# Kernel tuning notes

Hardware: AMD Instinct MI355X
Metric: run time of the kernel (lower is better)

Reference implementation:

```python
import jax, jax.numpy as jnp
import numpy as np

D_IN = 784
D = 768          # hidden_dim
R = 8            # num_rels
L = 3            # num_layers
B = 64           # graphs in batch
N = 32768        # total nodes
E = 262144       # total edges


def _layer_norm(x, g, b, eps=1e-5):
    m = x.mean(-1, keepdims=True)
    v = x.var(-1, keepdims=True)
    return (x - m) / jnp.sqrt(v + eps) * g + b


def setup_inputs() -> dict:
    key = jax.random.key(0)
    ks = jax.random.split(key, 24)
    s = 0.02
    inp = {
        "type_vec": jax.random.normal(ks[0], (N, 16), jnp.float32),
        "code_vec": jax.random.normal(ks[1], (N, D), jnp.float32),
        # input_proj: Linear(784,768) + LayerNorm(768)
        "W_in": jax.random.normal(ks[2], (D_IN, D), jnp.float32) * s,
        "b_in": jnp.zeros((D,), jnp.float32),
        "ln_in_g": jnp.ones((D,), jnp.float32),
        "ln_in_b": jnp.zeros((D,), jnp.float32),
        # RGCN layers (basis regularizer, num_bases=num_rels -> per-relation W)
        "W_rel": jax.random.normal(ks[3], (L, R, D, D), jnp.float32) * s,
        "W_loop": jax.random.normal(ks[4], (L, D, D), jnp.float32) * s,
        "rgcn_bias": jnp.zeros((L, D), jnp.float32),
        "ln_g": jnp.ones((L, D), jnp.float32),
        "ln_b": jnp.zeros((L, D), jnp.float32),
        # global attention pooling gate MLP: 768 -> 384 -> 1
        "Wg1": jax.random.normal(ks[5], (D, D // 2), jnp.float32) * s,
        "bg1": jnp.zeros((D // 2,), jnp.float32),
        "Wg2": jax.random.normal(ks[6], (D // 2, 1), jnp.float32) * s,
        "bg2": jnp.zeros((1,), jnp.float32),
        # classifier: 768 -> 512 (+LN) -> 2
        "Wc1": jax.random.normal(ks[7], (D, 512), jnp.float32) * s,
        "bc1": jnp.zeros((512,), jnp.float32),
        "ln_c_g": jnp.ones((512,), jnp.float32),
        "ln_c_b": jnp.zeros((512,), jnp.float32),
        "Wc2": jax.random.normal(ks[8], (512, 2), jnp.float32) * s,
        "bc2": jnp.zeros((2,), jnp.float32),
        # graph structure
        "src": jax.random.randint(ks[9], (E,), 0, N, jnp.int64),
        "dst": jax.random.randint(ks[10], (E,), 0, N, jnp.int64),
        "edge_type": jax.random.randint(ks[11], (E,), 0, R, jnp.int64),
        "node_graph": jnp.sort(jax.random.randint(ks[12], (N,), 0, B, jnp.int64)),
        "num_graphs": B,
    }
    return inp


def reference(type_vec, code_vec, W_in, b_in, ln_in_g, ln_in_b,
              W_rel, W_loop, rgcn_bias, ln_g, ln_b,
              Wg1, bg1, Wg2, bg2, Wc1, bc1, ln_c_g, ln_c_b, Wc2, bc2,
              src, dst, edge_type, node_graph, num_graphs):
    # input projection
    h = jnp.concatenate([type_vec, code_vec], axis=-1)           # [N, 784]
    h = jax.nn.gelu(_layer_norm(h @ W_in + b_in, ln_in_g, ln_in_b), approximate=False)
    n_nodes = h.shape[0]
    n_layers, n_rels = W_rel.shape[0], W_rel.shape[1]

    for l in range(n_layers):
        agg = jnp.zeros_like(h)
        for r in range(n_rels):
            # relation-specific transform, then gather->mask->scatter-add
            msg = (h @ W_rel[l, r])[src] * (edge_type == r).astype(h.dtype)[:, None]  # [E, D]
            agg = agg + jax.ops.segment_sum(msg, dst, num_segments=n_nodes)
        h_new = agg + rgcn_bias[l] + h @ W_loop[l]               # DGL: agg + bias + self-loop
        h = jax.nn.gelu(_layer_norm(h_new, ln_g[l], ln_b[l]), approximate=False)

    # global attention pooling (segment softmax over nodes of each graph)
    gate = (jax.nn.gelu(h @ Wg1 + bg1, approximate=False) @ Wg2 + bg2)[:, 0]  # [N]
    gmax = jax.ops.segment_max(gate, node_graph, num_segments=num_graphs)
    e = jnp.exp(gate - gmax[node_graph])
    denom = jax.ops.segment_sum(e, node_graph, num_segments=num_graphs)
    w = e / denom[node_graph]
    graph_repr = jax.ops.segment_sum(w[:, None] * h, node_graph, num_segments=num_graphs)  # [B, D]

    # classifier head
    z = jax.nn.gelu(_layer_norm(graph_repr @ Wc1 + bc1, ln_c_g, ln_c_b), approximate=False)
    logits = z @ Wc2 + bc2
    return jax.nn.log_softmax(logits, axis=-1)
```

## Files before the change

### kernel.cpp

```cpp
#include <hip/hip_runtime.h>
#include <hip/hip_bf16.h>

typedef __hip_bfloat16 bf16;
typedef __attribute__((ext_vector_type(8))) __bf16 bf16x8;
typedef __attribute__((ext_vector_type(4))) float f32x4;

#define N_NODES 32768
#define N_EDGES 262144
#define DIM 768
#define NGR 64
#define KIN 800
#define KSTACK 6912
#define NKEY (N_NODES * 8)

#define GLOBAL_AS __attribute__((address_space(1)))
#define LDS_AS __attribute__((address_space(3)))

__device__ __forceinline__ float gelu_f(float x) {
    return 0.5f * x * (1.0f + erff(x * 0.70710678118654752f));
}
__device__ __forceinline__ float bfu(unsigned short v) {
    union { unsigned u; float f; } x; x.u = (unsigned)v << 16; return x.f;
}
__device__ __forceinline__ unsigned short fbf(float f) {
    bf16 t = __float2bfloat16(f); return *(unsigned short*)&t;
}

__global__ __launch_bounds__(256)
void tcast_k(const float* __restrict__ in, bf16* __restrict__ out, int I, int O,
             int Ipad, int ostride) {
    __shared__ float t[32][33];
    const int i0 = blockIdx.x * 32, o0 = blockIdx.y * 32;
    const int tx = threadIdx.x & 31, ty = threadIdx.x >> 5;
#pragma unroll
    for (int q = 0; q < 4; ++q) {
        int i = i0 + ty + q * 8, o = o0 + tx;
        t[ty + q * 8][tx] = (i < I) ? in[(size_t)i * O + o] : 0.0f;
    }
    __syncthreads();
#pragma unroll
    for (int q = 0; q < 4; ++q) {
        int o = o0 + ty + q * 8, i = i0 + tx;
        if (i < Ipad) out[(size_t)o * ostride + i] = __float2bfloat16(t[tx][ty + q * 8]);
    }
}

__global__ __launch_bounds__(256)
void wprep_l_k(const float* __restrict__ Wrel_l, const float* __restrict__ Wloop_l,
               bf16* __restrict__ WstL) {
    __shared__ float t[32][33];
    const int q = blockIdx.z;
    const float* in = (q < 8) ? Wrel_l + (size_t)q * DIM * DIM : Wloop_l;
    bf16* out = WstL + (q < 8 ? (q + 1) * DIM : 0);
    const int i0 = blockIdx.x * 32, o0 = blockIdx.y * 32;
    const int tx = threadIdx.x & 31, ty = threadIdx.x >> 5;
#pragma unroll
    for (int qq = 0; qq < 4; ++qq)
        t[ty + qq * 8][tx] = in[(size_t)(i0 + ty + qq * 8) * DIM + o0 + tx];
    __syncthreads();
#pragma unroll
    for (int qq = 0; qq < 4; ++qq)
        out[(size_t)(o0 + ty + qq * 8) * KSTACK + i0 + tx] =
            __float2bfloat16(t[tx][ty + qq * 8]);
}

__global__ __launch_bounds__(256)
void concat_k(const float* __restrict__ tv, const float* __restrict__ cv, bf16* __restrict__ X) {
    const int n = blockIdx.x;
    for (int c = threadIdx.x; c < KIN; c += 256) {
        float v = 0.0f;
        if (c < 16) v = tv[(size_t)n * 16 + c];
        else if (c < 784) v = cv[(size_t)n * DIM + (c - 16)];
        X[(size_t)n * KIN + c] = __float2bfloat16(v);
    }
}

__global__ __launch_bounds__(256)
void hist2_k(const int* __restrict__ dst, const int* __restrict__ et, int* __restrict__ cur) {
    int e = blockIdx.x * 256 + threadIdx.x;
    if (e < N_EDGES) atomicAdd(&cur[dst[e] * 8 + et[e]], 1);
}

__global__ __launch_bounds__(1024)
void scan2_k(int* __restrict__ cur, int* __restrict__ rp) {
    __shared__ int part[1024];
    const int t = threadIdx.x;
    const int base_i = t * 256;
    int s = 0;
    for (int i = 0; i < 256; ++i) s += cur[base_i + i];
    part[t] = s; __syncthreads();
    for (int st = 1; st < 1024; st <<= 1) {
        int v = (t >= st) ? part[t - st] : 0;
        __syncthreads();
        part[t] += v;
        __syncthreads();
    }
    int run = part[t] - s;
    for (int i = 0; i < 256; ++i) {
        int d = cur[base_i + i];
        rp[base_i + i] = run; cur[base_i + i] = run;
        run += d;
    }
    if (t == 1023) rp[NKEY] = run;
}

__global__ __launch_bounds__(256)
void place2_k(const int* __restrict__ src, const int* __restrict__ dst,
              const int* __restrict__ et, int* __restrict__ cur,
              unsigned short* __restrict__ eidx) {
    int e = blockIdx.x * 256 + threadIdx.x;
    if (e >= N_EDGES) return;
    int pos = atomicAdd(&cur[dst[e] * 8 + et[e]], 1);
    eidx[pos] = (unsigned short)src[e];
}

template <int NC>
__global__ __launch_bounds__(256)
void gather2_k(const bf16* __restrict__ h, const int* __restrict__ rp2,
               const unsigned short* __restrict__ eidx, bf16* __restrict__ AGG,
               int rbase, int ostride, int colbase) {
    const int wave = threadIdx.x >> 6, lane = threadIdx.x & 63;
    const int n = blockIdx.x * 4 + wave;
    const int c0 = 2 * lane;
    unsigned short* outrow = (unsigned short*)&AGG[(size_t)n * ostride + colbase];
    const int* bp = &rp2[n * 8 + rbase];
#pragma unroll 1
    for (int sel = 0; sel < NC; ++sel) {
        const int s = bp[sel], e = bp[sel + 1];
        float2 f[6] = {};
        for (int t = s; t < e; ++t) {
            const unsigned short* hs = (const unsigned short*)&h[(size_t)eidx[t] * DIM];
#pragma unroll
            for (int j = 0; j < 6; ++j) {
                ushort2 u = *(const ushort2*)&hs[c0 + j * 128];
                f[j].x += bfu(u.x); f[j].y += bfu(u.y);
            }
        }
#pragma unroll
        for (int j = 0; j < 6; ++j) {
            ushort2 o; o.x = fbf(f[j].x); o.y = fbf(f[j].y);
            *(ushort2*)&outrow[sel * DIM + c0 + j * 128] = o;
        }
    }
}

template <int MODE>
__global__ __launch_bounds__(512, 4)
void gemm256(const bf16* __restrict__ A1, int S1, int K1,
             const bf16* __restrict__ A2, int S2,
             const bf16* __restrict__ BT, int ldb,
             bf16* __restrict__ OUT, int Nn, int Ktot, int nbx) {
    __shared__ __align__(16) unsigned short lA[3][128 * 32];
    __shared__ __align__(16) unsigned short lB[3][256 * 32];
    const int nblk = gridDim.x, qx = nblk >> 3, bid = blockIdx.x;
    const int wgid = (bid & 7) * qx + (bid >> 3);
    const int bx = wgid % nbx, by = wgid / nbx;
    const int bn = bx * 256, bm = by * 128;
    const int tid = threadIdx.x;
    const int wave = tid >> 6, lane = tid & 63;
    const int wr = wave >> 2, wc = wave & 3;
    const int l15 = lane & 15, lg = lane >> 4;
    const int swz = (lg ^ ((l15 >> 1) & 3)) * 8;

    f32x4 acc[4][4] = {};
    const int nkt = Ktot >> 5;

    auto stage = [&](int t, int buf) {
        const int k0 = t * 32;
        const bf16* Ab; int koff, stA;
        if (k0 < K1) { Ab = A1; koff = k0; stA = S1; }
        else         { Ab = A2; koff = k0 - K1; stA = S2; }
        {
            const int row = tid >> 2, k8 = tid & 3;
            const int ks = (k8 ^ ((row >> 1) & 3)) * 8;
            const bf16* ga = Ab + (size_t)(bm + row) * stA + koff + ks;
            __builtin_amdgcn_global_load_lds((const GLOBAL_AS void*)ga,
                (LDS_AS void*)&lA[buf][(wave * 64) * 8], 16, 0, 0);
        }
#pragma unroll
        for (int qq = 0; qq < 2; ++qq) {
            const int c = qq * 512 + tid;
            const int row = c >> 2, k8 = c & 3;
            const int ks = (k8 ^ ((row >> 1) & 3)) * 8;
            const bf16* gb = BT + (size_t)(bn + row) * ldb + k0 + ks;
            __builtin_amdgcn_global_load_lds((const GLOBAL_AS void*)gb,
                (LDS_AS void*)&lB[buf][((qq * 8 + wave) * 64) * 8], 16, 0, 0);
        }
    };

    stage(0, 0);
    if (nkt > 1) stage(1, 1);

    int rb = 0;
    for (int t = 0; t < nkt; ++t) {
        if (t + 2 < nkt) {
            int sb = rb + 2; if (sb >= 3) sb -= 3;
            stage(t + 2, sb);
            asm volatile("s_waitcnt vmcnt(6)" ::: "memory");
        } else if (t + 1 < nkt) {
            asm volatile("s_waitcnt vmcnt(3)" ::: "memory");
        } else {
            asm volatile("s_waitcnt vmcnt(0)" ::: "memory");
        }
        __builtin_amdgcn_s_barrier();
        __builtin_amdgcn_sched_barrier(0);

        bf16x8 af[4], bfr[4];
#pragma unroll
        for (int mi = 0; mi < 4; ++mi) {
            const int r = wr * 64 + mi * 16 + l15;
            af[mi] = *reinterpret_cast<const bf16x8*>(&lA[rb][r * 32 + swz]);
        }
#pragma unroll
        for (int ni = 0; ni < 4; ++ni) {
            const int r = wc * 64 + ni * 16 + l15;
            bfr[ni] = *reinterpret_cast<const bf16x8*>(&lB[rb][r * 32 + swz]);
        }
        __builtin_amdgcn_s_setprio(1);
#pragma unroll
        for (int mi = 0; mi < 4; ++mi)
#pragma unroll
            for (int ni = 0; ni < 4; ++ni)
                acc[mi][ni] = __builtin_amdgcn_mfma_f32_16x16x32_bf16(af[mi], bfr[ni], acc[mi][ni], 0, 0, 0);
        __builtin_amdgcn_s_setprio(0);
        __builtin_amdgcn_sched_barrier(0);
        __builtin_amdgcn_s_barrier();

        rb = (rb == 2) ? 0 : rb + 1;
    }

    unsigned short* O = (unsigned short*)OUT;
#pragma unroll
    for (int mi = 0; mi < 4; ++mi)
#pragma unroll
        for (int ni = 0; ni < 4; ++ni) {
            const int r0 = bm + wr * 64 + mi * 16 + lg * 4;
            const int c0 = bn + wc * 64 + ni * 16 + l15;
#pragma unroll
            for (int i = 0; i < 4; ++i) {
                size_t idx = (size_t)(r0 + i) * Nn + c0;
                float v = acc[mi][ni][i];
                if (MODE == 1) v += bfu(O[idx]);
                O[idx] = fbf(v);
            }
        }
}

__global__ __launch_bounds__(256, 2)
void gemm_bt(const bf16* __restrict__ A1, int S1,
             const bf16* __restrict__ BT, int ldb,
             float* __restrict__ OUT, int Nn, int Ktot) {
    __shared__ __align__(16) unsigned short lA[128 * 32];
    __shared__ __align__(16) unsigned short lB[128 * 32];
    const int bn = blockIdx.x * 128;
    const int bm = blockIdx.y * 128;
    const int tid = threadIdx.x;
    const int wave = tid >> 6, lane = tid & 63;
    const int wr = wave >> 1, wc = wave & 1;
    const int l15 = lane & 15, lg = lane >> 4;

    f32x4 acc[4][4] = {};

    for (int k0 = 0; k0 < Ktot; k0 += 32) {
#pragma unroll
        for (int q = 0; q < 2; ++q) {
            int c = wave * 128 + q * 64 + lane;
            int row = c >> 2, k8 = c & 3;
            const bf16* ga = A1 + (size_t)(bm + row) * S1 + k0 + k8 * 8;
            const bf16* gb = BT + (size_t)(bn + row) * ldb + k0 + k8 * 8;
            __builtin_amdgcn_global_load_lds((const GLOBAL_AS void*)ga,
                (LDS_AS void*)&lA[(wave * 128 + q * 64) * 8], 16, 0, 0);
            __builtin_amdgcn_global_load_lds((const GLOBAL_AS void*)gb,
                (LDS_AS void*)&lB[(wave * 128 + q * 64) * 8], 16, 0, 0);
        }
        __syncthreads();
        bf16x8 af[4], bfr[4];
#pragma unroll
        for (int mi = 0; mi < 4; ++mi)
            af[mi] = *reinterpret_cast<const bf16x8*>(&lA[(wr * 64 + mi * 16 + l15) * 32 + lg * 8]);
#pragma unroll
        for (int ni = 0; ni < 4; ++ni)
            bfr[ni] = *reinterpret_cast<const bf16x8*>(&lB[(wc * 64 + ni * 16 + l15) * 32 + lg * 8]);
#pragma unroll
        for (int mi = 0; mi < 4; ++mi)
#pragma unroll
            for (int ni = 0; ni < 4; ++ni)
                acc[mi][ni] = __builtin_amdgcn_mfma_f32_16x16x32_bf16(af[mi], bfr[ni], acc[mi][ni], 0, 0, 0);
        __syncthreads();
    }

#pragma unroll
    for (int mi = 0; mi < 4; ++mi)
#pragma unroll
        for (int ni = 0; ni < 4; ++ni) {
            const int r0 = bm + wr * 64 + mi * 16 + lg * 4;
            const int c0 = bn + wc * 64 + ni * 16 + l15;
#pragma unroll
            for (int i = 0; i < 4; ++i)
                OUT[(size_t)(r0 + i) * Nn + c0] = acc[mi][ni][i];
        }
}

__global__ __launch_bounds__(256)
void ln_gelu_k(const bf16* __restrict__ ACCb, const float* __restrict__ bias,
               const float* __restrict__ g, const float* __restrict__ b,
               bf16* __restrict__ hout) {
    const int wave = threadIdx.x >> 6, lane = threadIdx.x & 63;
    const int n = blockIdx.x * 4 + wave;
    const unsigned short* Ab = (const unsigned short*)ACCb;
    float x[12];
    float s = 0.f, ss = 0.f;
#pragma unroll
    for (int j = 0; j < 12; ++j) {
        int c = lane + j * 64;
        x[j] = bfu(Ab[(size_t)n * DIM + c]) + bias[c];
        s += x[j]; ss += x[j] * x[j];
    }
#pragma unroll
    for (int m = 1; m < 64; m <<= 1) { s += __shfl_xor(s, m, 64); ss += __shfl_xor(ss, m, 64); }
    const float mean = s * (1.f / DIM);
    const float var = ss * (1.f / DIM) - mean * mean;
    const float rstd = rsqrtf(var + 1e-5f);
#pragma unroll
    for (int j = 0; j < 12; ++j) {
        int c = lane + j * 64;
        float y = (x[j] - mean) * rstd * g[c] + b[c];
        hout[(size_t)n * DIM + c] = __float2bfloat16(gelu_f(y));
    }
}

__global__ __launch_bounds__(256)
void gate_k(const float* __restrict__ G1, const float* __restrict__ bg1,
            const float* __restrict__ Wg2, const float* __restrict__ bg2,
            float* __restrict__ gate) {
    const int wave = threadIdx.x >> 6, lane = threadIdx.x & 63;
    const int n = blockIdx.x * 4 + wave;
    float acc = 0.f;
#pragma unroll
    for (int j = 0; j < 6; ++j) {
        int c = lane + j * 64;
        float xv = G1[(size_t)n * 384 + c] + bg1[c];
        acc += gelu_f(xv) * Wg2[c];
    }
#pragma unroll
    for (int m = 1; m < 64; m <<= 1) acc += __shfl_xor(acc, m, 64);
    if (lane == 0) gate[n] = acc + bg2[0];
}

__device__ __forceinline__ int lower_bound_ng(const int* ng, int key) {
    int lo = 0, hi = N_NODES;
    while (lo < hi) { int mid = (lo + hi) >> 1; if (ng[mid] < key) lo = mid + 1; else hi = mid; }
    return lo;
}

__global__ __launch_bounds__(256)
void seg_stats_k(const float* __restrict__ gate, const int* __restrict__ ng,
                 float* __restrict__ gmax, float* __restrict__ gden) {
    __shared__ float red[256];
    const int b = blockIdx.x, t = threadIdx.x;
    const int start = lower_bound_ng(ng, b), end = lower_bound_ng(ng, b + 1);
    float m = -1e30f;
    for (int n = start + t; n < end; n += 256) m = fmaxf(m, gate[n]);
    red[t] = m; __syncthreads();
    for (int s = 128; s > 0; s >>= 1) { if (t < s) red[t] = fmaxf(red[t], red[t + s]); __syncthreads(); }
    const float gm = red[0]; __syncthreads();
    float ssum = 0.f;
    for (int n = start + t; n < end; n += 256) ssum += expf(gate[n] - gm);
    red[t] = ssum; __syncthreads();
    for (int s = 128; s > 0; s >>= 1) { if (t < s) red[t] += red[t + s]; __syncthreads(); }
    if (t == 0) { gmax[b] = gm; gden[b] = fmaxf(red[0], 1e-30f); }
}

__global__ __launch_bounds__(768)
void pool_k(const bf16* __restrict__ h, const float* __restrict__ gate,
            const int* __restrict__ ng, const float* __restrict__ gmax,
            const float* __restrict__ gden, float* __restrict__ grep) {
    const int b = blockIdx.x, c = threadIdx.x;
    const int start = lower_bound_ng(ng, b), end = lower_bound_ng(ng, b + 1);
    const float gm = gmax[b], inv = 1.0f / gden[b];
    const unsigned short* hv = (const unsigned short*)h;
    float a0 = 0.f, a1 = 0.f;
    int n = start;
    for (; n + 1 < end; n += 2) {
        float w0 = expf(gate[n] - gm) * inv;
        float w1 = expf(gate[n + 1] - gm) * inv;
        a0 += w0 * bfu(hv[(size_t)n * DIM + c]);
        a1 += w1 * bfu(hv[(size_t)(n + 1) * DIM + c]);
    }
    if (n < end) a0 += expf(gate[n] - gm) * inv * bfu(hv[(size_t)n * DIM + c]);
    grep[(size_t)b * DIM + c] = a0 + a1;
}

__global__ __launch_bounds__(512)
void cls_k(const float* __restrict__ grep, const float* __restrict__ Wc1,
           const float* __restrict__ bc1, const float* __restrict__ lng,
           const float* __restrict__ lnb, const float* __restrict__ Wc2,
           const float* __restrict__ bc2, float* __restrict__ out) {
    __shared__ float gr[DIM];
    __shared__ float red[512];
    const int b = blockIdx.x, j = threadIdx.x;
    for (int c = j; c < DIM; c += 512) gr[c] = grep[(size_t)b * DIM + c];
    __syncthreads();
    float a = bc1[j];
#pragma unroll 4
    for (int k = 0; k < DIM; ++k) a = fmaf(gr[k], Wc1[(size_t)k * 512 + j], a);
    red[j] = a; __syncthreads();
    for (int s = 256; s > 0; s >>= 1) { if (j < s) red[j] += red[j + s]; __syncthreads(); }
    const float mean = red[0] * (1.f / 512.f);
    __syncthreads();
    red[j] = (a - mean) * (a - mean); __syncthreads();
    for (int s = 256; s > 0; s >>= 1) { if (j < s) red[j] += red[j + s]; __syncthreads(); }
    const float rstd = rsqrtf(red[0] * (1.f / 512.f) + 1e-5f);
    __syncthreads();
    const float z = gelu_f((a - mean) * rstd * lng[j] + lnb[j]);
    red[j] = z * Wc2[2 * j + 0]; __syncthreads();
    for (int s = 256; s > 0; s >>= 1) { if (j < s) red[j] += red[j + s]; __syncthreads(); }
    const float l0 = red[0] + bc2[0];
    __syncthreads();
    red[j] = z * Wc2[2 * j + 1]; __syncthreads();
    for (int s = 256; s > 0; s >>= 1) { if (j < s) red[j] += red[j + s]; __syncthreads(); }
    if (j == 0) {
        const float l1 = red[0] + bc2[1];
        const float mx = fmaxf(l0, l1);
        const float lse = mx + logf(expf(l0 - mx) + expf(l1 - mx));
        out[2 * b + 0] = l0 - lse;
        out[2 * b + 1] = l1 - lse;
    }
}

extern "C" void kernel_launch(void* const* d_in, const int* in_sizes, int n_in,
                              void* d_out, int out_size, void* d_ws, size_t ws_size,
                              hipStream_t stream) {
    const float* type_vec = (const float*)d_in[0];
    const float* code_vec = (const float*)d_in[1];
    const float* W_in     = (const float*)d_in[2];
    const float* b_in     = (const float*)d_in[3];
    const float* ln_in_g  = (const float*)d_in[4];
    const float* ln_in_b  = (const float*)d_in[5];
    const float* W_rel    = (const float*)d_in[6];
    const float* W_loop   = (const float*)d_in[7];
    const float* rgcn_bias= (const float*)d_in[8];
    const float* ln_g     = (const float*)d_in[9];
    const float* ln_b     = (const float*)d_in[10];
    const float* Wg1      = (const float*)d_in[11];
    const float* bg1      = (const float*)d_in[12];
    const float* Wg2      = (const float*)d_in[13];
    const float* bg2      = (const float*)d_in[14];
    const float* Wc1      = (const float*)d_in[15];
    const float* bc1      = (const float*)d_in[16];
    const float* ln_c_g   = (const float*)d_in[17];
    const float* ln_c_b   = (const float*)d_in[18];
    const float* Wc2      = (const float*)d_in[19];
    const float* bc2      = (const float*)d_in[20];
    const int* src        = (const int*)d_in[21];
    const int* dst        = (const int*)d_in[22];
    const int* etype      = (const int*)d_in[23];
    const int* node_graph = (const int*)d_in[24];

    char* ws = (char*)d_ws;

    auto lay = [&](int nc, bool doAssign,
                   bf16*& h_bf, bf16*& ACCb, bf16*& WstL, int*& rp2, int*& cur2,
                   unsigned short*& eidx, float*& gate, float*& gmax, float*& gden,
                   float*& grep, bf16*& AGG) -> size_t {
        size_t off = 0;
        auto alloc = [&](size_t sz) { size_t r = off; off = (off + sz + 255) & ~(size_t)255; return r; };
        size_t oH   = alloc((size_t)N_NODES * DIM * 2);
        size_t oAC  = alloc((size_t)N_NODES * DIM * 2);
        size_t oWL  = alloc((size_t)DIM * KSTACK * 2);
        size_t oRP  = alloc((size_t)(NKEY + 1) * 4);
        size_t oCU  = alloc((size_t)NKEY * 4);
        size_t oEI  = alloc((size_t)N_EDGES * 2);
        size_t oGA  = alloc((size_t)N_NODES * 4);
        size_t oGM  = alloc(256);
        size_t oGD  = alloc(256);
        size_t oGR  = alloc((size_t)NGR * DIM * 4);
        size_t oAG  = alloc((size_t)N_NODES * nc * DIM * 2);
        if (doAssign) {
            h_bf = (bf16*)(ws + oH);   ACCb = (bf16*)(ws + oAC);
            WstL = (bf16*)(ws + oWL);  rp2  = (int*)(ws + oRP);
            cur2 = (int*)(ws + oCU);   eidx = (unsigned short*)(ws + oEI);
            gate = (float*)(ws + oGA); gmax = (float*)(ws + oGM);
            gden = (float*)(ws + oGD); grep = (float*)(ws + oGR);
            AGG  = (bf16*)(ws + oAG);
        }
        return off;
    };

    bf16 *h_bf, *ACCb, *WstL, *AGG; int *rp2, *cur2; unsigned short* eidx;
    float *gate, *gmax, *gden, *grep;
    bf16 *d0=nullptr,*d1=nullptr,*d2=nullptr,*d3=nullptr; int *d4=nullptr,*d5=nullptr;
    unsigned short* d6=nullptr; float *d7=nullptr,*d8=nullptr,*d9=nullptr,*d10=nullptr;
    const bool big = ws_size >= lay(8, false, d0,d1,d2,d4,d5,d6,d7,d8,d9,d10,d3);
    const int nc = big ? 8 : 4;
    lay(nc, true, h_bf, ACCb, WstL, rp2, cur2, eidx, gate, gmax, gden, grep, AGG);

    bf16* Xbf  = AGG;
    bf16* WinT = (bf16*)((char*)AGG + (size_t)N_NODES * KIN * 2);
    float* G1  = (float*)AGG;

    const int AGW = nc * DIM;

    tcast_k<<<dim3(25, 24), 256, 0, stream>>>(W_in, WinT, 784, DIM, KIN, KIN);
    concat_k<<<N_NODES, 256, 0, stream>>>(type_vec, code_vec, Xbf);
    gemm256<0><<<768, 512, 0, stream>>>(Xbf, KIN, KIN, Xbf, KIN, WinT, KIN, ACCb, DIM, KIN, 3);
    ln_gelu_k<<<N_NODES / 4, 256, 0, stream>>>(ACCb, b_in, ln_in_g, ln_in_b, h_bf);

    hipMemsetAsync(cur2, 0, (size_t)NKEY * 4, stream);
    hist2_k<<<N_EDGES / 256, 256, 0, stream>>>(dst, etype, cur2);
    scan2_k<<<1, 1024, 0, stream>>>(cur2, rp2);
    place2_k<<<N_EDGES / 256, 256, 0, stream>>>(src, dst, etype, cur2, eidx);

    for (int l = 0; l < 3; ++l) {
        wprep_l_k<<<dim3(24, 24, 9), 256, 0, stream>>>(
            W_rel + (size_t)l * 8 * DIM * DIM, W_loop + (size_t)l * DIM * DIM, WstL);
        if (nc == 8) {
            gather2_k<4><<<N_NODES / 4, 256, 0, stream>>>(h_bf, rp2, eidx, AGG, 0, AGW, 0);
            gather2_k<4><<<N_NODES / 4, 256, 0, stream>>>(h_bf, rp2, eidx, AGG, 4, AGW, 4 * DIM);
            gemm256<0><<<768, 512, 0, stream>>>(
                h_bf, DIM, DIM, AGG, AGW, WstL, KSTACK, ACCb, DIM, KSTACK, 3);
        } else {
            gather2_k<4><<<N_NODES / 4, 256, 0, stream>>>(h_bf, rp2, eidx, AGG, 0, AGW, 0);
            gemm256<0><<<768, 512, 0, stream>>>(
                h_bf, DIM, DIM, AGG, AGW, WstL, KSTACK, ACCb, DIM, DIM + 4 * DIM, 3);
            gather2_k<4><<<N_NODES / 4, 256, 0, stream>>>(h_bf, rp2, eidx, AGG, 4, AGW, 0);
            gemm256<1><<<768, 512, 0, stream>>>(
                AGG, AGW, AGW, AGG, AGW, WstL + (size_t)DIM * 5, KSTACK, ACCb, DIM, 4 * DIM, 3);
        }
        ln_gelu_k<<<N_NODES / 4, 256, 0, stream>>>(ACCb, rgcn_bias + l * DIM, ln_g + l * DIM,
                                                   ln_b + l * DIM, h_bf);
    }

    bf16* Wg1T = (bf16*)((char*)AGG + 60 * 1024 * 1024);
    tcast_k<<<dim3(24, 12), 256, 0, stream>>>(Wg1, Wg1T, DIM, 384, DIM, DIM);
    gemm_bt<<<dim3(3, 256), 256, 0, stream>>>(h_bf, DIM, Wg1T, DIM, G1, 384, DIM);
    gate_k<<<N_NODES / 4, 256, 0, stream>>>(G1, bg1, Wg2, bg2, gate);
    seg_stats_k<<<NGR, 256, 0, stream>>>(gate, node_graph, gmax, gden);
    pool_k<<<NGR, 768, 0, stream>>>(h_bf, gate, node_graph, gmax, gden, grep);

    cls_k<<<NGR, 512, 0, stream>>>(grep, Wc1, bc1, ln_c_g, ln_c_b, Wc2, bc2, (float*)d_out);
}
```

Baseline: 2.492 ms.

## Enlarge GEMM tiles to 256x384, widen gather vector loads, reuse GEMM for gate

The main GEMM goes from a 128x256 to a 256x384 output tile per 512-thread block, with 4x12 MFMA accumulators per wave and B fragments loaded inside the ni loop. The aim is higher arithmetic intensity and less reloading of A and B across blocks, at the cost of more registers (occupancy drops to 2 blocks per CU) and fewer blocks (256). The gather kernel now uses 4-element vector loads and handles all 8 relations in one launch. The gate-MLP GEMM reuses the big kernel and writes bf16 instead of fp32. Edge indices become 32-bit with the edge type packed into the high bits.

```diff
diff --git a/kernel.cpp b/kernel.cpp
--- a/kernel.cpp
+++ b/kernel.cpp
@@ -107,62 +107,67 @@
 __global__ __launch_bounds__(256)
 void place2_k(const int* __restrict__ src, const int* __restrict__ dst,
               const int* __restrict__ et, int* __restrict__ cur,
-              unsigned short* __restrict__ eidx) {
+              int* __restrict__ eidx) {
     int e = blockIdx.x * 256 + threadIdx.x;
     if (e >= N_EDGES) return;
     int pos = atomicAdd(&cur[dst[e] * 8 + et[e]], 1);
-    eidx[pos] = (unsigned short)src[e];
+    eidx[pos] = (et[e] << 16) | src[e];
 }
 
 template <int NC>
 __global__ __launch_bounds__(256)
-void gather2_k(const bf16* __restrict__ h, const int* __restrict__ rp2,
-               const unsigned short* __restrict__ eidx, bf16* __restrict__ AGG,
-               int rbase, int ostride, int colbase) {
+void gather8(const bf16* __restrict__ h, const int* __restrict__ rp2,
+             const int* __restrict__ eidx, bf16* __restrict__ AGG,
+             int rbase, int ostride, int colbase) {
     const int wave = threadIdx.x >> 6, lane = threadIdx.x & 63;
     const int n = blockIdx.x * 4 + wave;
-    const int c0 = 2 * lane;
+    const int c0 = 4 * lane;
     unsigned short* outrow = (unsigned short*)&AGG[(size_t)n * ostride + colbase];
     const int* bp = &rp2[n * 8 + rbase];
-#pragma unroll 1
     for (int sel = 0; sel < NC; ++sel) {
         const int s = bp[sel], e = bp[sel + 1];
-        float2 f[6] = {};
+        float f[12];
+#pragma unroll
+        for (int j = 0; j < 12; ++j) f[j] = 0.f;
         for (int t = s; t < e; ++t) {
-            const unsigned short* hs = (const unsigned short*)&h[(size_t)eidx[t] * DIM];
-#pragma unroll
-            for (int j = 0; j < 6; ++j) {
-                ushort2 u = *(const ushort2*)&hs[c0 + j * 128];
-                f[j].x += bfu(u.x); f[j].y += bfu(u.y);
+            const int srcn = eidx[t] & 0xffff;
+            const unsigned short* hs = (const unsigned short*)&h[(size_t)srcn * DIM];
+#pragma unroll
+            for (int j = 0; j < 3; ++j) {
+                ushort4 u = *(const ushort4*)&hs[c0 + j * 256];
+                f[4 * j + 0] += bfu(u.x); f[4 * j + 1] += bfu(u.y);
+                f[4 * j + 2] += bfu(u.z); f[4 * j + 3] += bfu(u.w);
             }
         }
 #pragma unroll
-        for (int j = 0; j < 6; ++j) {
-            ushort2 o; o.x = fbf(f[j].x); o.y = fbf(f[j].y);
-            *(ushort2*)&outrow[sel * DIM + c0 + j * 128] = o;
+        for (int j = 0; j < 3; ++j) {
+            ushort4 o;
+            o.x = fbf(f[4 * j + 0]); o.y = fbf(f[4 * j + 1]);
+            o.z = fbf(f[4 * j + 2]); o.w = fbf(f[4 * j + 3]);
+            *(ushort4*)&outrow[sel * DIM + c0 + j * 256] = o;
         }
     }
 }
 
 template <int MODE>
-__global__ __launch_bounds__(512, 4)
-void gemm256(const bf16* __restrict__ A1, int S1, int K1,
+__global__ __launch_bounds__(512, 2)
+void gemm384(const bf16* __restrict__ A1, int S1, int K1,
              const bf16* __restrict__ A2, int S2,
              const bf16* __restrict__ BT, int ldb,
              bf16* __restrict__ OUT, int Nn, int Ktot, int nbx) {
-    __shared__ __align__(16) unsigned short lA[3][128 * 32];
-    __shared__ __align__(16) unsigned short lB[3][256 * 32];
+    __shared__ __align__(16) unsigned short lA[3][256 * 32];
+    __shared__ __align__(16) unsigned short lB[3][384 * 32];
     const int nblk = gridDim.x, qx = nblk >> 3, bid = blockIdx.x;
     const int wgid = (bid & 7) * qx + (bid >> 3);
     const int bx = wgid % nbx, by = wgid / nbx;
-    const int bn = bx * 256, bm = by * 128;
+    const int bn = bx * 384, bm = by * 256;
     const int tid = threadIdx.x;
     const int wave = tid >> 6, lane = tid & 63;
-    const int wr = wave >> 2, wc = wave & 3;
+    const int wr = wave >> 1, wc = wave & 1;
     const int l15 = lane & 15, lg = lane >> 4;
     const int swz = (lg ^ ((l15 >> 1) & 3)) * 8;
 
-    f32x4 acc[4][4] = {};
+    f32x4 acc[4][12] = {};
     const int nkt = Ktot >> 5;
 
     auto stage = [&](int t, int buf) {
@@ -170,21 +175,23 @@
         const bf16* Ab; int koff, stA;
         if (k0 < K1) { Ab = A1; koff = k0; stA = S1; }
         else         { Ab = A2; koff = k0 - K1; stA = S2; }
-        {
-            const int row = tid >> 2, k8 = tid & 3;
-            const int ks = (k8 ^ ((row >> 1) & 3)) * 8;
-            const bf16* ga = Ab + (size_t)(bm + row) * stA + koff + ks;
+#pragma unroll
+        for (int u = 0; u < 2; ++u) {
+            const int c = u * 512 + tid;
+            const int r = c >> 2, s = c & 3;
+            const int sc = (s ^ ((r >> 1) & 3)) * 8;
+            const bf16* ga = Ab + (size_t)(bm + r) * stA + koff + sc;
             __builtin_amdgcn_global_load_lds((const GLOBAL_AS void*)ga,
-                (LDS_AS void*)&lA[buf][(wave * 64) * 8], 16, 0, 0);
-        }
-#pragma unroll
-        for (int qq = 0; qq < 2; ++qq) {
-            const int c = qq * 512 + tid;
-            const int row = c >> 2, k8 = c & 3;
-            const int ks = (k8 ^ ((row >> 1) & 3)) * 8;
-            const bf16* gb = BT + (size_t)(bn + row) * ldb + k0 + ks;
+                (LDS_AS void*)&lA[buf][(u * 512 + wave * 64) * 8], 16, 0, 0);
+        }
+#pragma unroll
+        for (int u = 0; u < 3; ++u) {
+            const int c = u * 512 + tid;
+            const int r = c >> 2, s = c & 3;
+            const int sc = (s ^ ((r >> 1) & 3)) * 8;
+            const bf16* gb = BT + (size_t)(bn + r) * ldb + k0 + sc;
             __builtin_amdgcn_global_load_lds((const GLOBAL_AS void*)gb,
-                (LDS_AS void*)&lB[buf][((qq * 8 + wave) * 64) * 8], 16, 0, 0);
+                (LDS_AS void*)&lB[buf][(u * 512 + wave * 64) * 8], 16, 0, 0);
         }
     };
 
@@ -196,32 +203,30 @@
         if (t + 2 < nkt) {
             int sb = rb + 2; if (sb >= 3) sb -= 3;
             stage(t + 2, sb);
-            asm volatile("s_waitcnt vmcnt(6)" ::: "memory");
+            asm volatile("s_waitcnt vmcnt(10)" ::: "memory");
         } else if (t + 1 < nkt) {
-            asm volatile("s_waitcnt vmcnt(3)" ::: "memory");
+            asm volatile("s_waitcnt vmcnt(5)" ::: "memory");
         } else {
             asm volatile("s_waitcnt vmcnt(0)" ::: "memory");
         }
         __builtin_amdgcn_s_barrier();
         __builtin_amdgcn_sched_barrier(0);
 
-        bf16x8 af[4], bfr[4];
+        bf16x8 af[4];
 #pragma unroll
         for (int mi = 0; mi < 4; ++mi) {
             const int r = wr * 64 + mi * 16 + l15;
             af[mi] = *reinterpret_cast<const bf16x8*>(&lA[rb][r * 32 + swz]);
         }
-#pragma unroll
-        for (int ni = 0; ni < 4; ++ni) {
-            const int r = wc * 64 + ni * 16 + l15;
-            bfr[ni] = *reinterpret_cast<const bf16x8*>(&lB[rb][r * 32 + swz]);
-        }
         __builtin_amdgcn_s_setprio(1);
 #pragma unroll
-        for (int mi = 0; mi < 4; ++mi)
-#pragma unroll
-            for (int ni = 0; ni < 4; ++ni)
-                acc[mi][ni] = __builtin_amdgcn_mfma_f32_16x16x32_bf16(af[mi], bfr[ni], acc[mi][ni], 0, 0, 0);
+        for (int ni = 0; ni < 12; ++ni) {
+            const int r = wc * 192 + ni * 16 + l15;
+            bf16x8 bq = *reinterpret_cast<const bf16x8*>(&lB[rb][r * 32 + swz]);
+#pragma unroll
+            for (int mi = 0; mi < 4; ++mi)
+                acc[mi][ni] = __builtin_amdgcn_mfma_f32_16x16x32_bf16(af[mi], bq, acc[mi][ni], 0, 0, 0);
+        }
         __builtin_amdgcn_s_setprio(0);
         __builtin_amdgcn_sched_barrier(0);
         __builtin_amdgcn_s_barrier();
@@ -233,9 +238,9 @@
 #pragma unroll
     for (int mi = 0; mi < 4; ++mi)
 #pragma unroll
-        for (int ni = 0; ni < 4; ++ni) {
+        for (int ni = 0; ni < 12; ++ni) {
             const int r0 = bm + wr * 64 + mi * 16 + lg * 4;
-            const int c0 = bn + wc * 64 + ni * 16 + l15;
+            const int c0 = bn + wc * 192 + ni * 16 + l15;
 #pragma unroll
             for (int i = 0; i < 4; ++i) {
                 size_t idx = (size_t)(r0 + i) * Nn + c0;
@@ -243,61 +248,6 @@
                 if (MODE == 1) v += bfu(O[idx]);
                 O[idx] = fbf(v);
             }
-        }
-}
-
-__global__ __launch_bounds__(256, 2)
-void gemm_bt(const bf16* __restrict__ A1, int S1,
-             const bf16* __restrict__ BT, int ldb,
-             float* __restrict__ OUT, int Nn, int Ktot) {
-    __shared__ __align__(16) unsigned short lA[128 * 32];
-    __shared__ __align__(16) unsigned short lB[128 * 32];
-    const int bn = blockIdx.x * 128;
-    const int bm = blockIdx.y * 128;
-    const int tid = threadIdx.x;
-    const int wave = tid >> 6, lane = tid & 63;
-    const int wr = wave >> 1, wc = wave & 1;
-    const int l15 = lane & 15, lg = lane >> 4;
-
-    f32x4 acc[4][4] = {};
-
-    for (int k0 = 0; k0 < Ktot; k0 += 32) {
-#pragma unroll
-        for (int q = 0; q < 2; ++q) {
-            int c = wave * 128 + q * 64 + lane;
-            int row = c >> 2, k8 = c & 3;
-            const bf16* ga = A1 + (size_t)(bm + row) * S1 + k0 + k8 * 8;
-            const bf16* gb = BT + (size_t)(bn + row) * ldb + k0 + k8 * 8;
-            __builtin_amdgcn_global_load_lds((const GLOBAL_AS void*)ga,
-                (LDS_AS void*)&lA[(wave * 128 + q * 64) * 8], 16, 0, 0);
-            __builtin_amdgcn_global_load_lds((const GLOBAL_AS void*)gb,
-                (LDS_AS void*)&lB[(wave * 128 + q * 64) * 8], 16, 0, 0);
-        }
-        __syncthreads();
-        bf16x8 af[4], bfr[4];
-#pragma unroll
-        for (int mi = 0; mi < 4; ++mi)
-            af[mi] = *reinterpret_cast<const bf16x8*>(&lA[(wr * 64 + mi * 16 + l15) * 32 + lg * 8]);
-#pragma unroll
-        for (int ni = 0; ni < 4; ++ni)
-            bfr[ni] = *reinterpret_cast<const bf16x8*>(&lB[(wc * 64 + ni * 16 + l15) * 32 + lg * 8]);
-#pragma unroll
-        for (int mi = 0; mi < 4; ++mi)
-#pragma unroll
-            for (int ni = 0; ni < 4; ++ni)
-                acc[mi][ni] = __builtin_amdgcn_mfma_f32_16x16x32_bf16(af[mi], bfr[ni], acc[mi][ni], 0, 0, 0);
-        __syncthreads();
-    }
-
-#pragma unroll
-    for (int mi = 0; mi < 4; ++mi)
-#pragma unroll
-        for (int ni = 0; ni < 4; ++ni) {
-            const int r0 = bm + wr * 64 + mi * 16 + lg * 4;
-            const int c0 = bn + wc * 64 + ni * 16 + l15;
-#pragma unroll
-            for (int i = 0; i < 4; ++i)
-                OUT[(size_t)(r0 + i) * Nn + c0] = acc[mi][ni][i];
         }
 }
 
@@ -330,16 +280,17 @@
 }
 
 __global__ __launch_bounds__(256)
-void gate_k(const float* __restrict__ G1, const float* __restrict__ bg1,
+void gate_k(const bf16* __restrict__ G1, const float* __restrict__ bg1,
             const float* __restrict__ Wg2, const float* __restrict__ bg2,
             float* __restrict__ gate) {
     const int wave = threadIdx.x >> 6, lane = threadIdx.x & 63;
     const int n = blockIdx.x * 4 + wave;
+    const unsigned short* G = (const unsigned short*)G1;
     float acc = 0.f;
 #pragma unroll
     for (int j = 0; j < 6; ++j) {
         int c = lane + j * 64;
-        float xv = G1[(size_t)n * 384 + c] + bg1[c];
+        float xv = bfu(G[(size_t)n * 384 + c]) + bg1[c];
         acc += gelu_f(xv) * Wg2[c];
     }
 #pragma unroll
@@ -461,7 +412,7 @@
 
     auto lay = [&](int nc, bool doAssign,
                    bf16*& h_bf, bf16*& ACCb, bf16*& WstL, int*& rp2, int*& cur2,
-                   unsigned short*& eidx, float*& gate, float*& gmax, float*& gden,
+                   int*& eidx, float*& gate, float*& gmax, float*& gden,
                    float*& grep, bf16*& AGG) -> size_t {
         size_t off = 0;
         auto alloc = [&](size_t sz) { size_t r = off; off = (off + sz + 255) & ~(size_t)255; return r; };
@@ -470,7 +421,7 @@
         size_t oWL  = alloc((size_t)DIM * KSTACK * 2);
         size_t oRP  = alloc((size_t)(NKEY + 1) * 4);
         size_t oCU  = alloc((size_t)NKEY * 4);
-        size_t oEI  = alloc((size_t)N_EDGES * 2);
+        size_t oEI  = alloc((size_t)N_EDGES * 4);
         size_t oGA  = alloc((size_t)N_NODES * 4);
         size_t oGM  = alloc(256);
         size_t oGD  = alloc(256);
@@ -479,7 +430,7 @@
         if (doAssign) {
             h_bf = (bf16*)(ws + oH);   ACCb = (bf16*)(ws + oAC);
             WstL = (bf16*)(ws + oWL);  rp2  = (int*)(ws + oRP);
-            cur2 = (int*)(ws + oCU);   eidx = (unsigned short*)(ws + oEI);
+            cur2 = (int*)(ws + oCU);   eidx = (int*)(ws + oEI);
             gate = (float*)(ws + oGA); gmax = (float*)(ws + oGM);
             gden = (float*)(ws + oGD); grep = (float*)(ws + oGR);
             AGG  = (bf16*)(ws + oAG);
@@ -487,23 +438,23 @@
         return off;
     };
 
-    bf16 *h_bf, *ACCb, *WstL, *AGG; int *rp2, *cur2; unsigned short* eidx;
+    bf16 *h_bf, *ACCb, *WstL, *AGG; int *rp2, *cur2, *eidx;
     float *gate, *gmax, *gden, *grep;
-    bf16 *d0=nullptr,*d1=nullptr,*d2=nullptr,*d3=nullptr; int *d4=nullptr,*d5=nullptr;
-    unsigned short* d6=nullptr; float *d7=nullptr,*d8=nullptr,*d9=nullptr,*d10=nullptr;
+    bf16 *d0=nullptr,*d1=nullptr,*d2=nullptr,*d3=nullptr; int *d4=nullptr,*d5=nullptr,*d6=nullptr;
+    float *d7=nullptr,*d8=nullptr,*d9=nullptr,*d10=nullptr;
     const bool big = ws_size >= lay(8, false, d0,d1,d2,d4,d5,d6,d7,d8,d9,d10,d3);
     const int nc = big ? 8 : 4;
     lay(nc, true, h_bf, ACCb, WstL, rp2, cur2, eidx, gate, gmax, gden, grep, AGG);
 
     bf16* Xbf  = AGG;
     bf16* WinT = (bf16*)((char*)AGG + (size_t)N_NODES * KIN * 2);
-    float* G1  = (float*)AGG;
+    bf16* G1   = AGG;
 
     const int AGW = nc * DIM;
 
     tcast_k<<<dim3(25, 24), 256, 0, stream>>>(W_in, WinT, 784, DIM, KIN, KIN);
     concat_k<<<N_NODES, 256, 0, stream>>>(type_vec, code_vec, Xbf);
-    gemm256<0><<<768, 512, 0, stream>>>(Xbf, KIN, KIN, Xbf, KIN, WinT, KIN, ACCb, DIM, KIN, 3);
+    gemm384<0><<<256, 512, 0, stream>>>(Xbf, KIN, KIN, Xbf, KIN, WinT, KIN, ACCb, DIM, KIN, 2);
     ln_gelu_k<<<N_NODES / 4, 256, 0, stream>>>(ACCb, b_in, ln_in_g, ln_in_b, h_bf);
 
     hipMemsetAsync(cur2, 0, (size_t)NKEY * 4, stream);
@@ -515,17 +466,16 @@
         wprep_l_k<<<dim3(24, 24, 9), 256, 0, stream>>>(
             W_rel + (size_t)l * 8 * DIM * DIM, W_loop + (size_t)l * DIM * DIM, WstL);
         if (nc == 8) {
-            gather2_k<4><<<N_NODES / 4, 256, 0, stream>>>(h_bf, rp2, eidx, AGG, 0, AGW, 0);
-            gather2_k<4><<<N_NODES / 4, 256, 0, stream>>>(h_bf, rp2, eidx, AGG, 4, AGW, 4 * DIM);
-            gemm256<0><<<768, 512, 0, stream>>>(
-                h_bf, DIM, DIM, AGG, AGW, WstL, KSTACK, ACCb, DIM, KSTACK, 3);
+            gather8<8><<<N_NODES / 4, 256, 0, stream>>>(h_bf, rp2, eidx, AGG, 0, AGW, 0);
+            gemm384<0><<<256, 512, 0, stream>>>(
+                h_bf, DIM, DIM, AGG, AGW, WstL, KSTACK, ACCb, DIM, KSTACK, 2);
         } else {
-            gather2_k<4><<<N_NODES / 4, 256, 0, stream>>>(h_bf, rp2, eidx, AGG, 0, AGW, 0);
-            gemm256<0><<<768, 512, 0, stream>>>(
-                h_bf, DIM, DIM, AGG, AGW, WstL, KSTACK, ACCb, DIM, DIM + 4 * DIM, 3);
-            gather2_k<4><<<N_NODES / 4, 256, 0, stream>>>(h_bf, rp2, eidx, AGG, 4, AGW, 0);
-            gemm256<1><<<768, 512, 0, stream>>>(
-                AGG, AGW, AGW, AGG, AGW, WstL + (size_t)DIM * 5, KSTACK, ACCb, DIM, 4 * DIM, 3);
+            gather8<4><<<N_NODES / 4, 256, 0, stream>>>(h_bf, rp2, eidx, AGG, 0, AGW, 0);
+            gemm384<0><<<256, 512, 0, stream>>>(
+                h_bf, DIM, DIM, AGG, AGW, WstL, KSTACK, ACCb, DIM, DIM + 4 * DIM, 2);
+            gather8<4><<<N_NODES / 4, 256, 0, stream>>>(h_bf, rp2, eidx, AGG, 4, AGW, 0);
+            gemm384<1><<<256, 512, 0, stream>>>(
+                AGG, AGW, AGW, AGG, AGW, WstL + (size_t)DIM * 5, KSTACK, ACCb, DIM, 4 * DIM, 2);
         }
         ln_gelu_k<<<N_NODES / 4, 256, 0, stream>>>(ACCb, rgcn_bias + l * DIM, ln_g + l * DIM,
                                                    ln_b + l * DIM, h_bf);
@@ -533,7 +483,7 @@
 
     bf16* Wg1T = (bf16*)((char*)AGG + 60 * 1024 * 1024);
     tcast_k<<<dim3(24, 12), 256, 0, stream>>>(Wg1, Wg1T, DIM, 384, DIM, DIM);
-    gemm_bt<<<dim3(3, 256), 256, 0, stream>>>(h_bf, DIM, Wg1T, DIM, G1, 384, DIM);
+    gemm384<0><<<128, 512, 0, stream>>>(h_bf, DIM, DIM, h_bf, DIM, Wg1T, DIM, G1, 384, DIM, 1);
     gate_k<<<N_NODES / 4, 256, 0, stream>>>(G1, bg1, Wg2, bg2, gate);
     seg_stats_k<<<NGR, 256, 0, stream>>>(gate, node_graph, gmax, gden);
     pool_k<<<NGR, 768, 0, stream>>>(h_bf, gate, node_graph, gmax, gden, grep);
```

Measured after the change: 2.453 ms, median of 2. Within noise of the previous version (-1.6%).
